# Kernel tuning notes

Measured on AMD Instinct MI355X. Metric: run time of the kernel, lower is better.

The kernel has to match this reference:

```python
import jax, jax.numpy as jnp
import numpy as np

HEADS = 16
ROPE_BASE = 10000.0


def _apply_rope(x, shift=0):
    # x: [b, h, s, d]; pairs (2i, 2i+1) form complex numbers rotated by m*theta_i
    b, h, s, d = x.shape
    half = d // 2
    theta = jnp.exp(-jnp.log(ROPE_BASE) * jnp.arange(0, d, 2, dtype=jnp.float32) / d)  # [half]
    m = jnp.arange(shift, shift + s, dtype=jnp.float32)[:, None]                        # [s,1]
    freqs = m * theta[None, :]                                                          # [s,half]
    cos = jnp.cos(freqs)[None, None]                                                    # [1,1,s,half]
    sin = jnp.sin(freqs)[None, None]
    xr = x.reshape(b, h, s, half, 2)
    xe, xo = xr[..., 0], xr[..., 1]
    oe = xe * cos - xo * sin
    oo = xe * sin + xo * cos
    return jnp.stack([oe, oo], axis=-1).reshape(b, h, s, d)


def setup_inputs() -> dict:
    key = jax.random.key(0)
    ks = jax.random.split(key, 4)
    b, s, dim = 2, 2048, 2048
    x = jax.random.normal(ks[0], (b, s, dim), dtype=jnp.float32)
    Wq = jax.random.normal(ks[1], (dim, dim), dtype=jnp.float32) * 0.02
    Wk = jax.random.normal(ks[2], (dim, dim), dtype=jnp.float32) * 0.02
    Wv = jax.random.normal(ks[3], (dim, dim), dtype=jnp.float32) * 0.02
    return {"x": x, "Wq": Wq, "Wk": Wk, "Wv": Wv}


def reference(x, Wq, Wk, Wv):
    b, s, dim = x.shape
    h = HEADS
    d = dim // h
    # QKV projections (torch Linear: y = x @ W^T), split into heads: b h s d
    q = jnp.einsum('bsm,nm->bsn', x, Wq).reshape(b, s, h, d).transpose(0, 2, 1, 3)
    k = jnp.einsum('bsm,nm->bsn', x, Wk).reshape(b, s, h, d).transpose(0, 2, 1, 3)
    v = jnp.einsum('bsm,nm->bsn', x, Wv).reshape(b, s, h, d).transpose(0, 2, 1, 3)
    # RoPE (torch version is under no_grad -> detached)
    q = jax.lax.stop_gradient(_apply_rope(q.astype(jnp.float32)))
    k = jax.lax.stop_gradient(_apply_rope(k.astype(jnp.float32)))
    # causal scaled dot-product attention, fp32 softmax
    scale = 1.0 / jnp.sqrt(jnp.float32(d))
    scores = jnp.einsum('bhqd,bhkd->bhqk', q, k).astype(jnp.float32) * scale
    causal = jnp.tril(jnp.ones((s, s), dtype=bool))
    scores = jnp.where(causal[None, None], scores, jnp.float32(-1e30))
    attn = jax.nn.softmax(scores, axis=-1)
    out = jnp.einsum('bhqk,bhkd->bhqd', attn, v.astype(jnp.float32))
    # b h s d -> b s (h d)
    return out.transpose(0, 2, 1, 3).reshape(b, s, dim)
```

## Files before the change

### kernel.cpp

```cpp
#include <hip/hip_runtime.h>
#include <hip/hip_bf16.h>
#include <stdint.h>

typedef __bf16 bf16;
typedef bf16 bf16x8 __attribute__((ext_vector_type(8)));
typedef bf16 bf16x4 __attribute__((ext_vector_type(4)));
typedef float f32x4 __attribute__((ext_vector_type(4)));

#define MFMA16(a, b, c) __builtin_amdgcn_mfma_f32_16x16x32_bf16(a, b, c, 0, 0, 0)

static __device__ __forceinline__ bf16 f2b(float f) { return (bf16)f; }
static __device__ __forceinline__ float b2f(bf16 v) { return (float)v; }

static __device__ __forceinline__ void gload16(const void* src, void* dst) {
    __builtin_amdgcn_global_load_lds(
        (const __attribute__((address_space(1))) uint32_t*)src,
        (__attribute__((address_space(3))) uint32_t*)dst, 16, 0, 0);
}

__global__ void cvt_all(const float* __restrict__ x,  const float* __restrict__ wq,
                        const float* __restrict__ wk, const float* __restrict__ wv,
                        bf16* __restrict__ xb,  bf16* __restrict__ wqb,
                        bf16* __restrict__ wkb, bf16* __restrict__ wvb) {
    int i = blockIdx.x * blockDim.x + threadIdx.x;
    const float* src; bf16* dst; int off;
    if (i < 2097152)      { src = x;  dst = xb;  off = i; }
    else if (i < 3145728) { src = wq; dst = wqb; off = i - 2097152; }
    else if (i < 4194304) { src = wk; dst = wkb; off = i - 3145728; }
    else                  { src = wv; dst = wvb; off = i - 4194304; }
    float4 v = reinterpret_cast<const float4*>(src)[off];
    bf16x4 o;
    o[0] = f2b(v.x); o[1] = f2b(v.y); o[2] = f2b(v.z); o[3] = f2b(v.w);
    reinterpret_cast<bf16x4*>(dst)[off] = o;
}

__global__ void rope_table(float2* __restrict__ tbl) {
    int t = blockIdx.x * blockDim.x + threadIdx.x;
    int i = t & 63;
    int s = t >> 6;
    float theta = expf(-9.210340371976184f * (float)(2 * i) * (1.0f / 128.0f));
    float freq = (float)s * theta;
    float sv, cv;
    sincosf(freq, &sv, &cv);
    tbl[t] = make_float2(cv, sv);
}

__global__ __launch_bounds__(256) void gemm_qkv(const bf16* __restrict__ X,
                                                const bf16* __restrict__ Wq,
                                                const bf16* __restrict__ Wk,
                                                const bf16* __restrict__ Wv,
                                                bf16* __restrict__ Qm,
                                                bf16* __restrict__ Km,
                                                bf16* __restrict__ Vt,
                                                const float2* __restrict__ tbl) {
    const int K = 2048;
    __shared__ bf16 As[128 * 64];
    __shared__ bf16 Bs[128 * 64];

    const int z = blockIdx.z;
    const bf16* W = (z == 0) ? Wq : (z == 1) ? Wk : Wv;

    const int tid  = threadIdx.x;
    const int lane = tid & 63;
    const int w    = tid >> 6;
    const int wr   = (w >> 1) * 64;
    const int wc   = (w & 1) * 64;
    const int l15  = lane & 15;
    const int l4   = lane >> 4;
    const int rbase = blockIdx.x * 128;
    const int cbase = blockIdx.y * 128;

    const int srow = lane >> 3;
    const int sslot = lane & 7;

    f32x4 acc[4][4] = {};

    for (int kt = 0; kt < K; kt += 64) {
        __syncthreads();
#pragma unroll
        for (int i = 0; i < 4; ++i) {
            int c   = w * 4 + i;
            int row = c * 8 + srow;
            int gsl = sslot ^ (row & 7);
            gload16(&X[(size_t)(rbase + row) * K + kt + gsl * 8], (char*)As + c * 1024);
            gload16(&W[(size_t)(cbase + row) * K + kt + gsl * 8], (char*)Bs + c * 1024);
        }
        __syncthreads();

        bf16x8 af[2][4], bfr[2][4];
#pragma unroll
        for (int ks = 0; ks < 2; ++ks) {
#pragma unroll
            for (int mi = 0; mi < 4; ++mi) {
                int r    = wr + mi * 16 + l15;
                int phys = (ks * 4 + l4) ^ (r & 7);
                af[ks][mi] = *reinterpret_cast<const bf16x8*>((char*)As + r * 128 + phys * 16);
            }
#pragma unroll
            for (int ni = 0; ni < 4; ++ni) {
                int r    = wc + ni * 16 + l15;
                int phys = (ks * 4 + l4) ^ (r & 7);
                bfr[ks][ni] = *reinterpret_cast<const bf16x8*>((char*)Bs + r * 128 + phys * 16);
            }
        }
#pragma unroll
        for (int ks = 0; ks < 2; ++ks)
#pragma unroll
            for (int mi = 0; mi < 4; ++mi)
#pragma unroll
                for (int ni = 0; ni < 4; ++ni)
                    acc[mi][ni] = MFMA16(af[ks][mi], bfr[ks][ni], acc[mi][ni]);
    }

    if (z < 2) {
        bf16* Y = (z == 0) ? Qm : Km;
        const float scale = (z == 0) ? 0.1275174396094198f : 1.0f;
        const int odd = l15 & 1;
#pragma unroll
        for (int mi = 0; mi < 4; ++mi) {
            int r0 = rbase + wr + mi * 16 + l4 * 4;
#pragma unroll
            for (int i = 0; i < 4; ++i) {
                int r = r0 + i;
                int b = r >> 11, s = r & 2047;
#pragma unroll
                for (int ni = 0; ni < 4; ++ni) {
                    int n = cbase + wc + ni * 16 + l15;
                    int h = n >> 7, d = n & 127;
                    float v = acc[mi][ni][i];
                    float p = __shfl_xor(v, 1);
                    float2 cs = tbl[(s << 6) + (d >> 1)];
                    float res = v * cs.x + (odd ? p : -p) * cs.y;
                    Y[(((size_t)b * 16 + h) * 2048 + s) * 128 + d] = f2b(res * scale);
                }
            }
        }
    } else {
#pragma unroll
        for (int mi = 0; mi < 4; ++mi) {
            int r0 = rbase + wr + mi * 16 + l4 * 4;
            int b = r0 >> 11, s = r0 & 2047;
#pragma unroll
            for (int ni = 0; ni < 4; ++ni) {
                int n = cbase + wc + ni * 16 + l15;
                int h = n >> 7, d = n & 127;
                bf16x4 o;
#pragma unroll
                for (int i = 0; i < 4; ++i) o[i] = f2b(acc[mi][ni][i]);
                *reinterpret_cast<bf16x4*>(&Vt[(((size_t)b * 16 + h) * 128 + d) * 2048 + s]) = o;
            }
        }
    }
}

__global__ __launch_bounds__(256) void flash_attn(const bf16* __restrict__ Q,
                                                  const bf16* __restrict__ Km,
                                                  const bf16* __restrict__ Vt,
                                                  float* __restrict__ out) {
    __shared__ bf16 Ksh[64 * 128];
    __shared__ bf16 Vsh[128 * 64];
    __shared__ bf16 Psh[4][16 * 64];

    const int tid  = threadIdx.x;
    const int lane = tid & 63;
    const int w    = tid >> 6;
    const int l15  = lane & 15;
    const int l4   = lane >> 4;

    const int bx  = blockIdx.x;
    const int g   = (bx >> 5) & 7;
    const int seg = bx >> 8;
    const int qt  = (seg == 0) ? 31 - g : (seg == 1) ? g : (seg == 2) ? 23 - g : 8 + g;
    const int bh  = bx & 31;
    const int b   = bh >> 4, h = bh & 15;

    const bf16* Qb = Q  + (size_t)bh * 2048 * 128;
    const bf16* Kb = Km + (size_t)bh * 2048 * 128;
    const bf16* Vb = Vt + (size_t)bh * 128 * 2048;
    const int rw = qt * 64 + w * 16;

    auto stage = [&](int kvb) {
#pragma unroll
        for (int c4 = 0; c4 < 4; ++c4) {
            int c  = w * 4 + c4;
            int kr = c * 4 + (lane >> 4);
            int ks = (lane & 15) ^ (kr & 7);
            gload16((const char*)Kb + ((size_t)(kvb + kr) * 128 + ks * 8) * 2,
                    (char*)Ksh + c * 1024);
            int vr = c * 8 + (lane >> 3);
            int vs = (lane & 7) ^ (vr & 7);
            gload16((const char*)Vb + ((size_t)vr * 2048 + kvb + vs * 8) * 2,
                    (char*)Vsh + c * 1024);
        }
    };

    bf16x8 qf[4];
#pragma unroll
    for (int ks = 0; ks < 4; ++ks)
        qf[ks] = *reinterpret_cast<const bf16x8*>(
            &Qb[(size_t)(rw + l15) * 128 + ks * 32 + l4 * 8]);

    f32x4 o[8] = {};
    float mrow[4], lrow[4];
#pragma unroll
    for (int i = 0; i < 4; ++i) { mrow[i] = -1e30f; lrow[i] = 0.0f; }

    char* pw = (char*)Psh[w];

    for (int t = 0; t <= qt; ++t) {
        const int kvb = t * 64;
        __syncthreads();
        stage(kvb);
        __syncthreads();

        const char* kb = (const char*)Ksh;
        f32x4 sacc[4] = {};
        __builtin_amdgcn_s_setprio(1);
#pragma unroll
        for (int ns = 0; ns < 4; ++ns) {
            int r = ns * 16 + l15;
#pragma unroll
            for (int ks = 0; ks < 4; ++ks) {
                int phys = (ks * 4 + l4) ^ (r & 7);
                bf16x8 kf = *reinterpret_cast<const bf16x8*>(kb + r * 256 + phys * 16);
                sacc[ns] = MFMA16(qf[ks], kf, sacc[ns]);
            }
        }
        __builtin_amdgcn_s_setprio(0);

        if (t == qt) {
#pragma unroll
            for (int ns = 0; ns < 4; ++ns) {
                int col = kvb + ns * 16 + l15;
#pragma unroll
                for (int i = 0; i < 4; ++i) {
                    int row = rw + l4 * 4 + i;
                    if (col > row) sacc[ns][i] = -1e30f;
                }
            }
        }
#pragma unroll
        for (int i = 0; i < 4; ++i) {
            float sm = fmaxf(fmaxf(sacc[0][i], sacc[1][i]), fmaxf(sacc[2][i], sacc[3][i]));
            sm = fmaxf(sm, __shfl_xor(sm, 1));
            sm = fmaxf(sm, __shfl_xor(sm, 2));
            sm = fmaxf(sm, __shfl_xor(sm, 4));
            sm = fmaxf(sm, __shfl_xor(sm, 8));
            float nm    = fmaxf(mrow[i], sm);
            float alpha = __builtin_amdgcn_exp2f(mrow[i] - nm);
            mrow[i] = nm;
            float ps = 0.0f;
            int r = l4 * 4 + i;
            int f = r & 7;
#pragma unroll
            for (int ns = 0; ns < 4; ++ns) {
                float p = __builtin_amdgcn_exp2f(sacc[ns][i] - nm);
                ps += p;
                int col  = ns * 16 + l15;
                int slot = (col >> 3) ^ f;
                *(bf16*)(pw + r * 128 + slot * 16 + (col & 7) * 2) = f2b(p);
            }
            ps += __shfl_xor(ps, 1);
            ps += __shfl_xor(ps, 2);
            ps += __shfl_xor(ps, 4);
            ps += __shfl_xor(ps, 8);
            lrow[i] = lrow[i] * alpha + ps;
#pragma unroll
            for (int ds = 0; ds < 8; ++ds) o[ds][i] *= alpha;
        }
        asm volatile("s_waitcnt lgkmcnt(0)" ::: "memory");
        __builtin_amdgcn_sched_barrier(0);
        const char* vb = (const char*)Vsh;
        __builtin_amdgcn_s_setprio(1);
#pragma unroll
        for (int k2 = 0; k2 < 2; ++k2) {
            int pr   = l15;
            int phys = (k2 * 4 + l4) ^ (pr & 7);
            bf16x8 pa = *reinterpret_cast<const bf16x8*>(pw + pr * 128 + phys * 16);
#pragma unroll
            for (int ds = 0; ds < 8; ++ds) {
                int d     = ds * 16 + l15;
                int physv = (k2 * 4 + l4) ^ (d & 7);
                bf16x8 vf = *reinterpret_cast<const bf16x8*>(vb + d * 128 + physv * 16);
                o[ds] = MFMA16(pa, vf, o[ds]);
            }
        }
        __builtin_amdgcn_s_setprio(0);
    }

#pragma unroll
    for (int i = 0; i < 4; ++i) {
        float inv = 1.0f / lrow[i];
        int row = rw + l4 * 4 + i;
#pragma unroll
        for (int ds = 0; ds < 8; ++ds)
            out[((size_t)b * 2048 + row) * 2048 + h * 128 + ds * 16 + l15] = o[ds][i] * inv;
    }
}

extern "C" void kernel_launch(void* const* d_in, const int* in_sizes, int n_in,
                              void* d_out, int out_size, void* d_ws, size_t ws_size,
                              hipStream_t stream) {
    const float* x  = (const float*)d_in[0];
    const float* Wq = (const float*)d_in[1];
    const float* Wk = (const float*)d_in[2];
    const float* Wv = (const float*)d_in[3];
    float* out = (float*)d_out;
    char* ws = (char*)d_ws;

    bf16* xb   = (bf16*)(ws + 0);
    bf16* wqb  = (bf16*)(ws + 16777216);
    bf16* wkb  = (bf16*)(ws + 25165824);
    bf16* wvb  = (bf16*)(ws + 33554432);
    bf16* Qm   = (bf16*)(ws + 41943040);
    bf16* Km   = (bf16*)(ws + 58720256);
    bf16* Vt   = (bf16*)(ws + 75497472);
    float2* tbl = (float2*)(ws + 92274688);

    cvt_all<<<20480, 256, 0, stream>>>(x, Wq, Wk, Wv, xb, wqb, wkb, wvb);
    rope_table<<<512, 256, 0, stream>>>(tbl);

    dim3 gg(32, 16, 3);
    gemm_qkv<<<gg, 256, 0, stream>>>(xb, wqb, wkb, wvb, Qm, Km, Vt, tbl);

    flash_attn<<<1024, 256, 0, stream>>>(Qm, Km, Vt, out);
}
```

Baseline: 255.2 us.

## Restructure QKV GEMM into 256x128 double-buffered ping-pong pipeline with tile swizzle

The QKV projection GEMM moves from 128x128 tiles with 256 threads and a single LDS buffer to 256x128 tiles with 512 threads (8 waves), double-buffered LDS, and async global->LDS loads for the next tile issued between MFMA phases. Barriers bracket the MFMA phases and s_setprio is raised during them, so the waves interleave loads and math in ping-pong style. A 1D grid with a remapped block index improves L2 locality across tiles. The aim is to hide global load latency behind MFMA work, at the cost of a larger LDS footprint (96KB), more barriers, and fewer blocks in flight.

```diff
diff --git a/kernel.cpp b/kernel.cpp
--- a/kernel.cpp
+++ b/kernel.cpp
@@ -45,72 +45,139 @@
     tbl[t] = make_float2(cv, sv);
 }
 
-__global__ __launch_bounds__(256) void gemm_qkv(const bf16* __restrict__ X,
-                                                const bf16* __restrict__ Wq,
-                                                const bf16* __restrict__ Wk,
-                                                const bf16* __restrict__ Wv,
-                                                bf16* __restrict__ Qm,
-                                                bf16* __restrict__ Km,
-                                                bf16* __restrict__ Vt,
-                                                const float2* __restrict__ tbl) {
+__global__ __launch_bounds__(512, 2) void gemm_qkv(const bf16* __restrict__ X,
+                                                   const bf16* __restrict__ Wq,
+                                                   const bf16* __restrict__ Wk,
+                                                   const bf16* __restrict__ Wv,
+                                                   bf16* __restrict__ Qm,
+                                                   bf16* __restrict__ Km,
+                                                   bf16* __restrict__ Vt,
+                                                   const float2* __restrict__ tbl) {
     const int K = 2048;
-    __shared__ bf16 As[128 * 64];
-    __shared__ bf16 Bs[128 * 64];
-
-    const int z = blockIdx.z;
+    __shared__ bf16 As[2][256 * 64];
+    __shared__ bf16 Bs[2][128 * 64];
+
+    const int bid = blockIdx.x;
+    const int z = bid >> 8;
+    int j = bid & 255;
+    j = (j & 7) * 32 + (j >> 3);
+    const int mx = j >> 4, ny = j & 15;
+    const int rbase = mx * 256, cbase = ny * 128;
+
     const bf16* W = (z == 0) ? Wq : (z == 1) ? Wk : Wv;
 
     const int tid  = threadIdx.x;
     const int lane = tid & 63;
     const int w    = tid >> 6;
-    const int wr   = (w >> 1) * 64;
-    const int wc   = (w & 1) * 64;
+    const int wm   = w >> 1;
+    const int wn   = w & 1;
     const int l15  = lane & 15;
     const int l4   = lane >> 4;
-    const int rbase = blockIdx.x * 128;
-    const int cbase = blockIdx.y * 128;
-
-    const int srow = lane >> 3;
+
+    const int srow  = lane >> 3;
     const int sslot = lane & 7;
 
-    f32x4 acc[4][4] = {};
-
-    for (int kt = 0; kt < K; kt += 64) {
-        __syncthreads();
-#pragma unroll
-        for (int i = 0; i < 4; ++i) {
-            int c   = w * 4 + i;
+    auto stageA = [&](int buf, int tile, int h) {
+        int kt = tile * 64;
+#pragma unroll
+        for (int i = 0; i < 2; ++i) {
+            int c   = h * 16 + w * 2 + i;
             int row = c * 8 + srow;
             int gsl = sslot ^ (row & 7);
-            gload16(&X[(size_t)(rbase + row) * K + kt + gsl * 8], (char*)As + c * 1024);
-            gload16(&W[(size_t)(cbase + row) * K + kt + gsl * 8], (char*)Bs + c * 1024);
-        }
-        __syncthreads();
-
-        bf16x8 af[2][4], bfr[2][4];
-#pragma unroll
-        for (int ks = 0; ks < 2; ++ks) {
-#pragma unroll
-            for (int mi = 0; mi < 4; ++mi) {
-                int r    = wr + mi * 16 + l15;
-                int phys = (ks * 4 + l4) ^ (r & 7);
-                af[ks][mi] = *reinterpret_cast<const bf16x8*>((char*)As + r * 128 + phys * 16);
-            }
-#pragma unroll
-            for (int ni = 0; ni < 4; ++ni) {
-                int r    = wc + ni * 16 + l15;
-                int phys = (ks * 4 + l4) ^ (r & 7);
-                bfr[ks][ni] = *reinterpret_cast<const bf16x8*>((char*)Bs + r * 128 + phys * 16);
-            }
-        }
-#pragma unroll
-        for (int ks = 0; ks < 2; ++ks)
-#pragma unroll
-            for (int mi = 0; mi < 4; ++mi)
-#pragma unroll
-                for (int ni = 0; ni < 4; ++ni)
-                    acc[mi][ni] = MFMA16(af[ks][mi], bfr[ks][ni], acc[mi][ni]);
+            gload16(&X[(size_t)(rbase + row) * K + kt + gsl * 8],
+                    (char*)As[buf] + c * 1024);
+        }
+    };
+    auto stageB = [&](int buf, int tile, int h) {
+        int kt  = tile * 64;
+        int c   = h * 8 + w;
+        int row = c * 8 + srow;
+        int gsl = sslot ^ (row & 7);
+        gload16(&W[(size_t)(cbase + row) * K + kt + gsl * 8],
+                (char*)Bs[buf] + c * 1024);
+    };
+
+    auto rdA = [&](int buf, int mi, int ks) {
+        int r    = wm * 64 + mi * 16 + l15;
+        int phys = (ks * 4 + l4) ^ (r & 7);
+        return *reinterpret_cast<const bf16x8*>((char*)As[buf] + r * 128 + phys * 16);
+    };
+    auto rdB = [&](int buf, int ni, int ks) {
+        int r    = wn * 64 + ni * 16 + l15;
+        int phys = (ks * 4 + l4) ^ (r & 7);
+        return *reinterpret_cast<const bf16x8*>((char*)Bs[buf] + r * 128 + phys * 16);
+    };
+
+    f32x4 acc[4][4] = {};
+
+#define PHASE_OPEN                                                  \
+    __builtin_amdgcn_s_barrier();                                   \
+    asm volatile("s_waitcnt lgkmcnt(0)" ::: "memory");              \
+    __builtin_amdgcn_s_setprio(1)
+#define PHASE_CLOSE                                                 \
+    __builtin_amdgcn_s_setprio(0);                                  \
+    __builtin_amdgcn_s_barrier();                                   \
+    asm volatile("" ::: "memory")
+#define MFMA_QUAD(ar0, ar1, br0, br1, m0, m1, n0, n1)               \
+    acc[m0][n0] = MFMA16(ar0[0], br0[0], acc[m0][n0]);              \
+    acc[m0][n1] = MFMA16(ar0[0], br1[0], acc[m0][n1]);              \
+    acc[m1][n0] = MFMA16(ar1[0], br0[0], acc[m1][n0]);              \
+    acc[m1][n1] = MFMA16(ar1[0], br1[0], acc[m1][n1]);              \
+    acc[m0][n0] = MFMA16(ar0[1], br0[1], acc[m0][n0]);              \
+    acc[m0][n1] = MFMA16(ar0[1], br1[1], acc[m0][n1]);              \
+    acc[m1][n0] = MFMA16(ar1[1], br0[1], acc[m1][n0]);              \
+    acc[m1][n1] = MFMA16(ar1[1], br1[1], acc[m1][n1]);
+
+    stageA(0, 0, 0); stageB(0, 0, 0);
+    stageA(0, 0, 1); stageB(0, 0, 1);
+    stageA(1, 1, 0); stageB(1, 1, 0);
+    asm volatile("s_waitcnt vmcnt(3)" ::: "memory");
+    __builtin_amdgcn_s_barrier();
+    asm volatile("" ::: "memory");
+
+    for (int it = 0; it < 16; ++it) {
+        const int t1 = 2 * it + 1;
+        const int t2 = (2 * it + 2 < 32) ? 2 * it + 2 : 31;
+        const int t3 = (2 * it + 3 < 32) ? 2 * it + 3 : 31;
+        bf16x8 a0[2], a1[2], a2[2], a3[2], b0[2], b1[2], b2[2], b3[2];
+
+        a0[0] = rdA(0, 0, 0); a0[1] = rdA(0, 0, 1);
+        a1[0] = rdA(0, 1, 0); a1[1] = rdA(0, 1, 1);
+        b0[0] = rdB(0, 0, 0); b0[1] = rdB(0, 0, 1);
+        b1[0] = rdB(0, 1, 0); b1[1] = rdB(0, 1, 1);
+        stageA(1, t1, 1); stageB(1, t1, 1);
+        PHASE_OPEN; MFMA_QUAD(a0, a1, b0, b1, 0, 1, 0, 1); PHASE_CLOSE;
+        b2[0] = rdB(0, 2, 0); b2[1] = rdB(0, 2, 1);
+        b3[0] = rdB(0, 3, 0); b3[1] = rdB(0, 3, 1);
+        PHASE_OPEN; MFMA_QUAD(a0, a1, b2, b3, 0, 1, 2, 3); PHASE_CLOSE;
+        a2[0] = rdA(0, 2, 0); a2[1] = rdA(0, 2, 1);
+        a3[0] = rdA(0, 3, 0); a3[1] = rdA(0, 3, 1);
+        PHASE_OPEN; MFMA_QUAD(a2, a3, b0, b1, 2, 3, 0, 1); PHASE_CLOSE;
+        stageA(0, t2, 0); stageB(0, t2, 0);
+        asm volatile("s_waitcnt vmcnt(3)" ::: "memory");
+        PHASE_OPEN; MFMA_QUAD(a2, a3, b2, b3, 2, 3, 2, 3); PHASE_CLOSE;
+
+        a0[0] = rdA(1, 0, 0); a0[1] = rdA(1, 0, 1);
+        a1[0] = rdA(1, 1, 0); a1[1] = rdA(1, 1, 1);
+        b0[0] = rdB(1, 0, 0); b0[1] = rdB(1, 0, 1);
+        b1[0] = rdB(1, 1, 0); b1[1] = rdB(1, 1, 1);
+        stageA(0, t2, 1); stageB(0, t2, 1);
+        PHASE_OPEN; MFMA_QUAD(a0, a1, b0, b1, 0, 1, 0, 1); PHASE_CLOSE;
+        b2[0] = rdB(1, 2, 0); b2[1] = rdB(1, 2, 1);
+        b3[0] = rdB(1, 3, 0); b3[1] = rdB(1, 3, 1);
+        PHASE_OPEN; MFMA_QUAD(a0, a1, b2, b3, 0, 1, 2, 3); PHASE_CLOSE;
+        a2[0] = rdA(1, 2, 0); a2[1] = rdA(1, 2, 1);
+        a3[0] = rdA(1, 3, 0); a3[1] = rdA(1, 3, 1);
+        PHASE_OPEN; MFMA_QUAD(a2, a3, b0, b1, 2, 3, 0, 1); PHASE_CLOSE;
+        stageA(1, t3, 0); stageB(1, t3, 0);
+        asm volatile("s_waitcnt vmcnt(3)" ::: "memory");
+        PHASE_OPEN; MFMA_QUAD(a2, a3, b2, b3, 2, 3, 2, 3); PHASE_CLOSE;
     }
+#undef PHASE_OPEN
+#undef PHASE_CLOSE
+#undef MFMA_QUAD
+
+    asm volatile("s_waitcnt vmcnt(0)" ::: "memory");
 
     if (z < 2) {
         bf16* Y = (z == 0) ? Qm : Km;
@@ -118,14 +185,14 @@
         const int odd = l15 & 1;
 #pragma unroll
         for (int mi = 0; mi < 4; ++mi) {
-            int r0 = rbase + wr + mi * 16 + l4 * 4;
+            int r0 = rbase + wm * 64 + mi * 16 + l4 * 4;
 #pragma unroll
             for (int i = 0; i < 4; ++i) {
                 int r = r0 + i;
                 int b = r >> 11, s = r & 2047;
 #pragma unroll
                 for (int ni = 0; ni < 4; ++ni) {
-                    int n = cbase + wc + ni * 16 + l15;
+                    int n = cbase + wn * 64 + ni * 16 + l15;
                     int h = n >> 7, d = n & 127;
                     float v = acc[mi][ni][i];
                     float p = __shfl_xor(v, 1);
@@ -138,11 +205,11 @@
     } else {
 #pragma unroll
         for (int mi = 0; mi < 4; ++mi) {
-            int r0 = rbase + wr + mi * 16 + l4 * 4;
+            int r0 = rbase + wm * 64 + mi * 16 + l4 * 4;
             int b = r0 >> 11, s = r0 & 2047;
 #pragma unroll
             for (int ni = 0; ni < 4; ++ni) {
-                int n = cbase + wc + ni * 16 + l15;
+                int n = cbase + wn * 64 + ni * 16 + l15;
                 int h = n >> 7, d = n & 127;
                 bf16x4 o;
 #pragma unroll
@@ -320,8 +387,7 @@
     cvt_all<<<20480, 256, 0, stream>>>(x, Wq, Wk, Wv, xb, wqb, wkb, wvb);
     rope_table<<<512, 256, 0, stream>>>(tbl);
 
-    dim3 gg(32, 16, 3);
-    gemm_qkv<<<gg, 256, 0, stream>>>(xb, wqb, wkb, wvb, Qm, Km, Vt, tbl);
+    gemm_qkv<<<768, 512, 0, stream>>>(xb, wqb, wkb, wvb, Qm, Km, Vt, tbl);
 
     flash_attn<<<1024, 256, 0, stream>>>(Qm, Km, Vt, out);
 }
```

Result: faster. 249.2 us (-2.3%).

## Restructure QKV GEMM into 128x256 tiles with double-buffered LDS pipeline

Applied to the files above, without the earlier changes.

The QKV projection GEMM moves from 128x128 tiles with 256 threads to 128x256 tiles with 512 threads and double-buffered LDS. Global-to-LDS loads for the next k-tile are interleaved with MFMA phases using explicit waitcnt, barriers and setprio. It also remaps 1D block ids so that each XCD gets a contiguous chunk of work. The goal is to hide load latency and improve L2 reuse, at the cost of more LDS per block, higher register pressure, and hand-tuned vmcnt counts that must match the staging exactly.

```diff
diff --git a/kernel.cpp b/kernel.cpp
--- a/kernel.cpp
+++ b/kernel.cpp
@@ -45,73 +45,138 @@
     tbl[t] = make_float2(cv, sv);
 }
 
-__global__ __launch_bounds__(256) void gemm_qkv(const bf16* __restrict__ X,
-                                                const bf16* __restrict__ Wq,
-                                                const bf16* __restrict__ Wk,
-                                                const bf16* __restrict__ Wv,
-                                                bf16* __restrict__ Qm,
-                                                bf16* __restrict__ Km,
-                                                bf16* __restrict__ Vt,
-                                                const float2* __restrict__ tbl) {
+__global__ __launch_bounds__(512, 2) void gemm_qkv(const bf16* __restrict__ X,
+                                                   const bf16* __restrict__ Wq,
+                                                   const bf16* __restrict__ Wk,
+                                                   const bf16* __restrict__ Wv,
+                                                   bf16* __restrict__ Qm,
+                                                   bf16* __restrict__ Km,
+                                                   bf16* __restrict__ Vt,
+                                                   const float2* __restrict__ tbl) {
     const int K = 2048;
-    __shared__ bf16 As[128 * 64];
-    __shared__ bf16 Bs[128 * 64];
-
-    const int z = blockIdx.z;
+    __shared__ bf16 As[2][128 * 64];
+    __shared__ bf16 Bs[2][256 * 64];
+
+    const int bid = blockIdx.x;
+    const int wg  = (bid & 7) * 96 + (bid >> 3);
+    const int z   = wg >> 8;
+    const int t   = wg & 255;
+    const int rbase = (t >> 3) * 128;
+    const int cbase = (t & 7) * 256;
+
     const bf16* W = (z == 0) ? Wq : (z == 1) ? Wk : Wv;
 
     const int tid  = threadIdx.x;
     const int lane = tid & 63;
     const int w    = tid >> 6;
-    const int wr   = (w >> 1) * 64;
-    const int wc   = (w & 1) * 64;
+    const int wm   = w >> 2;
+    const int wn   = w & 3;
     const int l15  = lane & 15;
     const int l4   = lane >> 4;
-    const int rbase = blockIdx.x * 128;
-    const int cbase = blockIdx.y * 128;
-
-    const int srow = lane >> 3;
+    const int srow  = lane >> 3;
     const int sslot = lane & 7;
 
-    f32x4 acc[4][4] = {};
-
-    for (int kt = 0; kt < K; kt += 64) {
-        __syncthreads();
-#pragma unroll
-        for (int i = 0; i < 4; ++i) {
-            int c   = w * 4 + i;
+    auto stageA = [&](int buf, int tile) {
+#pragma unroll
+        for (int i = 0; i < 2; ++i) {
+            int c   = w * 2 + i;
             int row = c * 8 + srow;
             int gsl = sslot ^ (row & 7);
-            gload16(&X[(size_t)(rbase + row) * K + kt + gsl * 8], (char*)As + c * 1024);
-            gload16(&W[(size_t)(cbase + row) * K + kt + gsl * 8], (char*)Bs + c * 1024);
-        }
-        __syncthreads();
-
-        bf16x8 af[2][4], bfr[2][4];
-#pragma unroll
-        for (int ks = 0; ks < 2; ++ks) {
-#pragma unroll
-            for (int mi = 0; mi < 4; ++mi) {
-                int r    = wr + mi * 16 + l15;
-                int phys = (ks * 4 + l4) ^ (r & 7);
-                af[ks][mi] = *reinterpret_cast<const bf16x8*>((char*)As + r * 128 + phys * 16);
-            }
-#pragma unroll
-            for (int ni = 0; ni < 4; ++ni) {
-                int r    = wc + ni * 16 + l15;
-                int phys = (ks * 4 + l4) ^ (r & 7);
-                bfr[ks][ni] = *reinterpret_cast<const bf16x8*>((char*)Bs + r * 128 + phys * 16);
-            }
-        }
-#pragma unroll
-        for (int ks = 0; ks < 2; ++ks)
-#pragma unroll
-            for (int mi = 0; mi < 4; ++mi)
-#pragma unroll
-                for (int ni = 0; ni < 4; ++ni)
-                    acc[mi][ni] = MFMA16(af[ks][mi], bfr[ks][ni], acc[mi][ni]);
-    }
-
+            gload16(&X[(size_t)(rbase + row) * K + tile * 64 + gsl * 8],
+                    (char*)As[buf] + c * 1024);
+        }
+    };
+    auto stageB1 = [&](int buf, int tile) {
+        int c   = w;
+        int row = c * 8 + srow;
+        int gsl = sslot ^ (row & 7);
+        gload16(&W[(size_t)(cbase + row) * K + tile * 64 + gsl * 8],
+                (char*)Bs[buf] + c * 1024);
+    };
+    auto stageB2 = [&](int buf, int tile) {
+#pragma unroll
+        for (int i = 0; i < 3; ++i) {
+            int c   = 8 + w * 3 + i;
+            int row = c * 8 + srow;
+            int gsl = sslot ^ (row & 7);
+            gload16(&W[(size_t)(cbase + row) * K + tile * 64 + gsl * 8],
+                    (char*)Bs[buf] + c * 1024);
+        }
+    };
+    auto rdA = [&](int buf, int mi, int ks) {
+        int r    = wm * 64 + mi * 16 + l15;
+        int phys = (ks * 4 + l4) ^ (r & 7);
+        return *reinterpret_cast<const bf16x8*>((char*)As[buf] + r * 128 + phys * 16);
+    };
+    auto rdB = [&](int buf, int ni, int ks) {
+        int r    = wn * 64 + ni * 16 + l15;
+        int phys = (ks * 4 + l4) ^ (r & 7);
+        return *reinterpret_cast<const bf16x8*>((char*)Bs[buf] + r * 128 + phys * 16);
+    };
+
+    f32x4 acc[4][4] = {};
+    bf16x8 aa[4][2], b0[2], b1[2], b2[2], b3[2];
+
+#define OPEN_PHASE                                              \
+    __builtin_amdgcn_s_barrier();                               \
+    asm volatile("s_waitcnt lgkmcnt(0)" ::: "memory");          \
+    __builtin_amdgcn_sched_barrier(0);                          \
+    __builtin_amdgcn_s_setprio(1)
+#define CLOSE_PHASE                                             \
+    __builtin_amdgcn_s_setprio(0);                              \
+    __builtin_amdgcn_s_barrier();                               \
+    asm volatile("" ::: "memory")
+#define QUAD(B0, B1, C0, C1)                                    \
+    _Pragma("unroll")                                           \
+    for (int ks = 0; ks < 2; ++ks) {                            \
+        _Pragma("unroll")                                       \
+        for (int mi = 0; mi < 4; ++mi) {                        \
+            acc[mi][C0] = MFMA16(aa[mi][ks], B0[ks], acc[mi][C0]); \
+            acc[mi][C1] = MFMA16(aa[mi][ks], B1[ks], acc[mi][C1]); \
+        }                                                       \
+    }
+#define LOAD_TILE(BUF)                                          \
+    _Pragma("unroll")                                           \
+    for (int mi = 0; mi < 4; ++mi) {                            \
+        aa[mi][0] = rdA(BUF, mi, 0); aa[mi][1] = rdA(BUF, mi, 1); \
+    }                                                           \
+    b0[0] = rdB(BUF, 0, 0); b0[1] = rdB(BUF, 0, 1);             \
+    b1[0] = rdB(BUF, 1, 0); b1[1] = rdB(BUF, 1, 1);             \
+    b2[0] = rdB(BUF, 2, 0); b2[1] = rdB(BUF, 2, 1);             \
+    b3[0] = rdB(BUF, 3, 0); b3[1] = rdB(BUF, 3, 1);
+
+    stageA(0, 0); stageB1(0, 0); stageB2(0, 0);
+    stageA(1, 1); stageB1(1, 1);
+    asm volatile("s_waitcnt vmcnt(3)" ::: "memory");
+    __builtin_amdgcn_s_barrier();
+    asm volatile("" ::: "memory");
+
+    for (int it = 0; it < 16; ++it) {
+        const int e  = 2 * it, o = e + 1;
+        const int e2 = (e + 2 < 32) ? e + 2 : 30;
+        const int o2 = (o + 2 < 32) ? o + 2 : 31;
+
+        LOAD_TILE(0);
+        stageB2(1, o);
+        OPEN_PHASE; QUAD(b0, b1, 0, 1); CLOSE_PHASE;
+        stageA(0, e2); stageB1(0, e2);
+        asm volatile("s_waitcnt vmcnt(3)" ::: "memory");
+        OPEN_PHASE; QUAD(b2, b3, 2, 3); CLOSE_PHASE;
+        LOAD_TILE(1);
+        stageB2(0, e2);
+        OPEN_PHASE; QUAD(b0, b1, 0, 1); CLOSE_PHASE;
+        stageA(1, o2); stageB1(1, o2);
+        asm volatile("s_waitcnt vmcnt(3)" ::: "memory");
+        OPEN_PHASE; QUAD(b2, b3, 2, 3); CLOSE_PHASE;
+    }
+#undef OPEN_PHASE
+#undef CLOSE_PHASE
+#undef QUAD
+#undef LOAD_TILE
+
+    asm volatile("s_waitcnt vmcnt(0)" ::: "memory");
+
+    const int wr = wm * 64, wc = wn * 64;
     if (z < 2) {
         bf16* Y = (z == 0) ? Qm : Km;
         const float scale = (z == 0) ? 0.1275174396094198f : 1.0f;
@@ -320,8 +385,7 @@
     cvt_all<<<20480, 256, 0, stream>>>(x, Wq, Wk, Wv, xb, wqb, wkb, wvb);
     rope_table<<<512, 256, 0, stream>>>(tbl);
 
-    dim3 gg(32, 16, 3);
-    gemm_qkv<<<gg, 256, 0, stream>>>(xb, wqb, wkb, wvb, Qm, Km, Vt, tbl);
+    gemm_qkv<<<768, 512, 0, stream>>>(xb, wqb, wkb, wvb, Qm, Km, Vt, tbl);
 
     flash_attn<<<1024, 256, 0, stream>>>(Qm, Km, Vt, out);
 }
```

Measured after the change: 240.5 us. 5.8% less time.
